# Optimization experiments

Hardware: AMD Instinct MI355X
Metric: run time of the kernel (lower is better)

## Reference

```python
import jax, jax.numpy as jnp
import numpy as np

B, N, L, S, H, E, D = 4, 32, 256, 256, 8, 64, 64

def setup_inputs() -> dict:
    key = jax.random.key(0)
    k1, k2, k3, k4 = jax.random.split(key, 4)
    queries = jax.random.normal(k1, (B, N, L, H, E), dtype=jnp.float32)
    keys = jax.random.normal(k2, (B, N, S, H, E), dtype=jnp.float32)
    values = jax.random.normal(k3, (B, N, S, H, D), dtype=jnp.float32)
    # additive causal mask [L, S]: 0 where allowed, -1e9 where masked
    causal = jnp.tril(jnp.ones((L, S), dtype=bool))
    attn_mask = jnp.where(causal, 0.0, -1e9).astype(jnp.float32)
    # cross-layer accumulated prior scores [B, N, H, L, S]
    attn_scores = jax.random.normal(k4, (B, N, H, L, S), dtype=jnp.float32) * 0.1
    query_lengths = jnp.full((B,), L, dtype=jnp.int32)
    key_lengths = jnp.full((B,), S, dtype=jnp.int32)
    return {"queries": queries, "keys": keys, "values": values,
            "attn_mask": attn_mask, "attn_scores": attn_scores,
            "query_lengths": query_lengths, "key_lengths": key_lengths}

def reference(queries, keys, values, attn_mask, attn_scores, query_lengths, key_lengths):
    # queries: [B,N,L,H,E], keys: [B,N,S,H,E], values: [B,N,S,H,D]
    e = queries.shape[-1]
    softmax_temp = 1.0 / np.sqrt(e).astype(np.float32)
    QK = jnp.einsum('bnlhe,bnshe->bnhls', queries, keys)
    # additive mask broadcast over [B,N,H]
    scores = QK + attn_mask + attn_scores  # accumulated scores returned for next layer
    A = jax.nn.softmax(softmax_temp * scores, axis=-1)  # dropout omitted (eval mode)
    V = jnp.einsum('bnhls,bnshd->bnlhd', A, values)
    return scores, V
```

## Files before the change

### kernel.cpp

```cpp
#include <hip/hip_runtime.h>
#include <stdint.h>


typedef __attribute__((ext_vector_type(8))) short bfrag;
typedef __attribute__((ext_vector_type(4))) float f32x4;
typedef __attribute__((ext_vector_type(4))) int i32x4;

__device__ __forceinline__ uint32_t f2bf(float f) {
  uint32_t u = __builtin_bit_cast(uint32_t, f);
  return (u + 0x7FFFu + ((u >> 16) & 1u)) >> 16;
}
__device__ __forceinline__ uint32_t pk(float a, float b) {
  return f2bf(a) | (f2bf(b) << 16);
}

#define MFMA(a, b, c) __builtin_amdgcn_mfma_f32_16x16x32_bf16((a), (b), (c), 0, 0, 0)

__global__ __launch_bounds__(1024, 2) void attn_kernel(
    const float* __restrict__ Qg, const float* __restrict__ Kg,
    const float* __restrict__ Vg, const float* __restrict__ Pg,
    float* __restrict__ Sc, float* __restrict__ Ov)
{
  __shared__ unsigned short Ks[256 * 72];
  __shared__ unsigned short Vt[64 * 266];

  const int bnh = blockIdx.x;
  const int bn = bnh >> 3, h = bnh & 7;
  const int t = threadIdx.x;

  {
    const int e0 = (t & 15) * 4;
    const int rb = t >> 4;
    const float* kp = Kg + (size_t)bn * 131072 + h * 64 + e0;
#pragma unroll
    for (int it = 0; it < 4; ++it) {
      const int r = it * 64 + rb;
      const f32x4 k4 = *(const f32x4*)(kp + (size_t)r * 512);
      uint2 kk;
      kk.x = pk(k4.x, k4.y);
      kk.y = pk(k4.z, k4.w);
      *(uint2*)(&Ks[r * 72 + e0]) = kk;
    }
  }
  {
    const int d = t & 63, sg = t >> 6;
    const float* vp = Vg + (size_t)bn * 131072 + h * 64 + d;
#pragma unroll
    for (int it = 0; it < 4; ++it) {
      const int sv = it * 64 + sg * 4;
      const float v0 = vp[(size_t)(sv + 0) * 512];
      const float v1 = vp[(size_t)(sv + 1) * 512];
      const float v2 = vp[(size_t)(sv + 2) * 512];
      const float v3 = vp[(size_t)(sv + 3) * 512];
      uint2 vv;
      vv.x = pk(v0, v1);
      vv.y = pk(v2, v3);
      *(uint2*)(&Vt[d * 266 + sv]) = vv;
    }
  }

  const int lane = t & 63;
  const int wave = t >> 6;
  const int ql = lane & 15;
  const int g  = lane >> 4;
  const int qbase = wave * 16;
  const int q = qbase + ql;
  const float temp = 0.125f;

  bfrag qf[2];
#pragma unroll
  for (int ks = 0; ks < 2; ++ks) {
    const float* qp = Qg + (size_t)bn * 131072 + (size_t)q * 512 + h * 64 + ks * 32 + g * 8;
    const f32x4 qa = *(const f32x4*)qp;
    const f32x4 qb = *(const f32x4*)(qp + 4);
    union { i32x4 i; bfrag b; } u;
    u.i = i32x4{(int)pk(qa.x, qa.y), (int)pk(qa.z, qa.w),
                (int)pk(qb.x, qb.y), (int)pk(qb.z, qb.w)};
    qf[ks] = u.b;
  }

  __syncthreads();

  f32x4 O[4];
#pragma unroll
  for (int ds = 0; ds < 4; ++ds) O[ds] = f32x4{0.f, 0.f, 0.f, 0.f};
  float m = -1e30f, lsum = 0.f;

  const size_t scb = (size_t)bnh << 16;
  const float* prp = Pg + scb + (size_t)q * 256 + 4 * g;
  float* scp = Sc + scb + (size_t)q * 256 + 4 * g;
  const int pvmax = wave >> 1;

  f32x4 pr0 = __builtin_nontemporal_load((const f32x4*)(prp));
  f32x4 pr1 = __builtin_nontemporal_load((const f32x4*)(prp + 16));

#pragma unroll 1
  for (int st = 0; st < 8; ++st) {
    const int s0 = st * 32;
    bfrag kf[2][2];
#pragma unroll
    for (int ss = 0; ss < 2; ++ss)
#pragma unroll
      for (int ks = 0; ks < 2; ++ks)
        kf[ss][ks] = *(const bfrag*)(&Ks[(s0 + 16 * ss + ql) * 72 + ks * 32 + g * 8]);

    f32x4 acc[2];
#pragma unroll
    for (int ss = 0; ss < 2; ++ss) {
      f32x4 a = f32x4{0.f, 0.f, 0.f, 0.f};
      a = MFMA(kf[ss][0], qf[0], a);
      a = MFMA(kf[ss][1], qf[1], a);
      const int sb = s0 + 16 * ss + 4 * g;
#pragma unroll
      for (int r = 0; r < 4; ++r)
        a[r] = (sb + r <= q) ? a[r] : a[r] - 1e9f;
      acc[ss] = a + (ss == 0 ? pr0 : pr1);
    }

    if (st < 7) {
      pr0 = __builtin_nontemporal_load((const f32x4*)(prp + (st + 1) * 32));
      pr1 = __builtin_nontemporal_load((const f32x4*)(prp + (st + 1) * 32 + 16));
    }

    __builtin_nontemporal_store(acc[0], (f32x4*)(scp + s0));
    __builtin_nontemporal_store(acc[1], (f32x4*)(scp + s0 + 16));

    if (st <= pvmax) {
      float tm = fmaxf(fmaxf(fmaxf(acc[0][0], acc[0][1]), fmaxf(acc[0][2], acc[0][3])),
                       fmaxf(fmaxf(acc[1][0], acc[1][1]), fmaxf(acc[1][2], acc[1][3])));
      tm = fmaxf(tm, __shfl_xor(tm, 16));
      tm = fmaxf(tm, __shfl_xor(tm, 32));
      tm *= temp;
      const float mnew = fmaxf(m, tm);
      const float fct = __expf(m - mnew);
      m = mnew;
      float p[8];
#pragma unroll
      for (int ss = 0; ss < 2; ++ss)
#pragma unroll
        for (int r = 0; r < 4; ++r)
          p[ss * 4 + r] = __expf(fmaf(temp, acc[ss][r], -mnew));
      float ts = (p[0] + p[1]) + (p[2] + p[3]) + (p[4] + p[5]) + (p[6] + p[7]);
      ts += __shfl_xor(ts, 16);
      ts += __shfl_xor(ts, 32);
      lsum = lsum * fct + ts;
#pragma unroll
      for (int ds = 0; ds < 4; ++ds) O[ds] *= fct;

      const int w0x = (int)pk(p[0], p[1]), w0y = (int)pk(p[2], p[3]);
      const int w1x = (int)pk(p[4], p[5]), w1y = (int)pk(p[6], p[7]);
      const int srcA = ((g & 1) << 5) + ql;
      const int a0 = __shfl(w0x, srcA),      a1 = __shfl(w1x, srcA);
      const int b0 = __shfl(w0y, srcA),      b1 = __shfl(w1y, srcA);
      const int c0 = __shfl(w0x, srcA + 16), c1 = __shfl(w1x, srcA + 16);
      const int d0 = __shfl(w0y, srcA + 16), d1 = __shfl(w1y, srcA + 16);
      union { i32x4 i; bfrag b; } pu;
      pu.i = i32x4{g < 2 ? a0 : a1, g < 2 ? b0 : b1,
                   g < 2 ? c0 : c1, g < 2 ? d0 : d1};

      bfrag vf[4];
#pragma unroll
      for (int ds = 0; ds < 4; ++ds)
        vf[ds] = *(const bfrag*)(&Vt[(16 * ds + ql) * 266 + s0 + g * 8]);
#pragma unroll
      for (int ds = 0; ds < 4; ++ds) O[ds] = MFMA(vf[ds], pu.b, O[ds]);
    }
  }

  {
    const float inv = 1.f / lsum;
    float* op = Ov + (size_t)bn * 131072 + (size_t)q * 512 + h * 64 + 4 * g;
#pragma unroll
    for (int ds = 0; ds < 4; ++ds) {
      f32x4 o = O[ds] * inv;
      *(f32x4*)(op + 16 * ds) = o;
    }
  }
}

extern "C" void kernel_launch(void* const* d_in, const int* in_sizes, int n_in,
                              void* d_out, int out_size, void* d_ws, size_t ws_size,
                              hipStream_t stream) {
  const float* Qg = (const float*)d_in[0];
  const float* Kg = (const float*)d_in[1];
  const float* Vg = (const float*)d_in[2];
  const float* Pg = (const float*)d_in[4];
  float* Sc = (float*)d_out;
  float* Ov = Sc + (size_t)4 * 32 * 8 * 256 * 256;
  attn_kernel<<<dim3(1024), dim3(1024), 0, stream>>>(Qg, Kg, Vg, Pg, Sc, Ov);
}
```

Baseline: 155.2 us.

## Stream K/V tiles through double-buffered swizzled LDS and balance causal waves

Replaces the up-front load of the full K and transposed V into large padded LDS arrays with per-step 32-row tiles. Each tile is converted to bf16 into a small double-buffered, XOR-swizzled LDS buffer while register prefetch fetches the next tile. A permutation table assigns query tiles to waves, and launch bounds are raised so far less LDS allows more resident blocks. This aims to hide global load latency behind compute and raise occupancy, at the cost of a barrier every iteration and tighter register limits.

New measurement: 288.2 us. 85.7% more time.

```diff
diff --git a/kernel.cpp b/kernel.cpp
--- a/kernel.cpp
+++ b/kernel.cpp
@@ -4,6 +4,7 @@
 
 typedef __attribute__((ext_vector_type(8))) short bfrag;
 typedef __attribute__((ext_vector_type(4))) float f32x4;
+typedef __attribute__((ext_vector_type(2))) float f32x2;
 typedef __attribute__((ext_vector_type(4))) int i32x4;
 
 __device__ __forceinline__ uint32_t f2bf(float f) {
@@ -16,56 +17,36 @@
 
 #define MFMA(a, b, c) __builtin_amdgcn_mfma_f32_16x16x32_bf16((a), (b), (c), 0, 0, 0)
 
-__global__ __launch_bounds__(1024, 2) void attn_kernel(
+__global__ __launch_bounds__(1024, 8) void attn_kernel(
     const float* __restrict__ Qg, const float* __restrict__ Kg,
     const float* __restrict__ Vg, const float* __restrict__ Pg,
     float* __restrict__ Sc, float* __restrict__ Ov)
 {
-  __shared__ unsigned short Ks[256 * 72];
-  __shared__ unsigned short Vt[64 * 266];
+  __shared__ char Kb[2][4096];
+  __shared__ char Vb[2][4096];
 
   const int bnh = blockIdx.x;
   const int bn = bnh >> 3, h = bnh & 7;
   const int t = threadIdx.x;
-
-  {
-    const int e0 = (t & 15) * 4;
-    const int rb = t >> 4;
-    const float* kp = Kg + (size_t)bn * 131072 + h * 64 + e0;
-#pragma unroll
-    for (int it = 0; it < 4; ++it) {
-      const int r = it * 64 + rb;
-      const f32x4 k4 = *(const f32x4*)(kp + (size_t)r * 512);
-      uint2 kk;
-      kk.x = pk(k4.x, k4.y);
-      kk.y = pk(k4.z, k4.w);
-      *(uint2*)(&Ks[r * 72 + e0]) = kk;
-    }
-  }
-  {
-    const int d = t & 63, sg = t >> 6;
-    const float* vp = Vg + (size_t)bn * 131072 + h * 64 + d;
-#pragma unroll
-    for (int it = 0; it < 4; ++it) {
-      const int sv = it * 64 + sg * 4;
-      const float v0 = vp[(size_t)(sv + 0) * 512];
-      const float v1 = vp[(size_t)(sv + 1) * 512];
-      const float v2 = vp[(size_t)(sv + 2) * 512];
-      const float v3 = vp[(size_t)(sv + 3) * 512];
-      uint2 vv;
-      vv.x = pk(v0, v1);
-      vv.y = pk(v2, v3);
-      *(uint2*)(&Vt[d * 266 + sv]) = vv;
-    }
-  }
-
   const int lane = t & 63;
   const int wave = t >> 6;
   const int ql = lane & 15;
   const int g  = lane >> 4;
-  const int qbase = wave * 16;
-  const int q = qbase + ql;
+  const int qt = (int)((0x783C96D25A1EB4F0ull >> (wave * 4)) & 15);
+  const int q = qt * 16 + ql;
+  const int pvmax = qt >> 1;
+  const int swzk = (ql & 7) << 4;
+  const int swzv = (ql & 3) << 4;
   const float temp = 0.125f;
+
+  const int kr_ = t >> 5;
+  const int kc_ = t & 31;
+  const int vd_ = t & 63;
+  const int vw_ = t >> 6;
+  const float* kgp = Kg + (size_t)bn * 131072 + h * 64 + (size_t)kr_ * 512 + 2 * kc_;
+  const float* vgp = Vg + (size_t)bn * 131072 + h * 64 + (size_t)(2 * vw_) * 512 + vd_;
+  const int kwoff = (kr_ * 128 + kc_ * 4) ^ ((kr_ & 7) << 4);
+  const int vwoff = (vd_ * 64 + vw_ * 4) ^ ((vd_ & 3) << 4);
 
   bfrag qf[2];
 #pragma unroll
@@ -79,7 +60,17 @@
     qf[ks] = u.b;
   }
 
-  __syncthreads();
+  f32x2 kreg = *(const f32x2*)kgp;
+  float vreg0 = vgp[0], vreg1 = vgp[512];
+  {
+    const uint32_t kk = pk(kreg[0], kreg[1]);
+    *(uint32_t*)(&Kb[0][0] + kwoff) = kk;
+    const uint32_t vv = pk(vreg0, vreg1);
+    *(uint32_t*)(&Vb[0][0] + vwoff) = vv;
+  }
+  kreg = *(const f32x2*)(kgp + 32 * 512);
+  vreg0 = vgp[16384];
+  vreg1 = vgp[16384 + 512];
 
   f32x4 O[4];
 #pragma unroll
@@ -89,20 +80,24 @@
   const size_t scb = (size_t)bnh << 16;
   const float* prp = Pg + scb + (size_t)q * 256 + 4 * g;
   float* scp = Sc + scb + (size_t)q * 256 + 4 * g;
-  const int pvmax = wave >> 1;
 
   f32x4 pr0 = __builtin_nontemporal_load((const f32x4*)(prp));
   f32x4 pr1 = __builtin_nontemporal_load((const f32x4*)(prp + 16));
+
+  asm volatile("s_waitcnt lgkmcnt(0)" ::: "memory");
+  __builtin_amdgcn_s_barrier();
 
 #pragma unroll 1
   for (int st = 0; st < 8; ++st) {
     const int s0 = st * 32;
+    const int p = (st & 1) << 12;
     bfrag kf[2][2];
 #pragma unroll
     for (int ss = 0; ss < 2; ++ss)
 #pragma unroll
       for (int ks = 0; ks < 2; ++ks)
-        kf[ss][ks] = *(const bfrag*)(&Ks[(s0 + 16 * ss + ql) * 72 + ks * 32 + g * 8]);
+        kf[ss][ks] = *(const bfrag*)(&Kb[0][0] + p +
+            (((16 * ss + ql) * 128 + ks * 64 + g * 16) ^ swzk));
 
     f32x4 acc[2];
 #pragma unroll
@@ -134,21 +129,21 @@
       const float mnew = fmaxf(m, tm);
       const float fct = __expf(m - mnew);
       m = mnew;
-      float p[8];
+      float pv[8];
 #pragma unroll
       for (int ss = 0; ss < 2; ++ss)
 #pragma unroll
         for (int r = 0; r < 4; ++r)
-          p[ss * 4 + r] = __expf(fmaf(temp, acc[ss][r], -mnew));
-      float ts = (p[0] + p[1]) + (p[2] + p[3]) + (p[4] + p[5]) + (p[6] + p[7]);
+          pv[ss * 4 + r] = __expf(fmaf(temp, acc[ss][r], -mnew));
+      float ts = (pv[0] + pv[1]) + (pv[2] + pv[3]) + (pv[4] + pv[5]) + (pv[6] + pv[7]);
       ts += __shfl_xor(ts, 16);
       ts += __shfl_xor(ts, 32);
       lsum = lsum * fct + ts;
 #pragma unroll
       for (int ds = 0; ds < 4; ++ds) O[ds] *= fct;
 
-      const int w0x = (int)pk(p[0], p[1]), w0y = (int)pk(p[2], p[3]);
-      const int w1x = (int)pk(p[4], p[5]), w1y = (int)pk(p[6], p[7]);
+      const int w0x = (int)pk(pv[0], pv[1]), w0y = (int)pk(pv[2], pv[3]);
+      const int w1x = (int)pk(pv[4], pv[5]), w1y = (int)pk(pv[6], pv[7]);
       const int srcA = ((g & 1) << 5) + ql;
       const int a0 = __shfl(w0x, srcA),      a1 = __shfl(w1x, srcA);
       const int b0 = __shfl(w0y, srcA),      b1 = __shfl(w1y, srcA);
@@ -161,10 +156,26 @@
       bfrag vf[4];
 #pragma unroll
       for (int ds = 0; ds < 4; ++ds)
-        vf[ds] = *(const bfrag*)(&Vt[(16 * ds + ql) * 266 + s0 + g * 8]);
+        vf[ds] = *(const bfrag*)(&Vb[0][0] + p +
+            (((16 * ds + ql) * 64 + g * 16) ^ swzv));
 #pragma unroll
       for (int ds = 0; ds < 4; ++ds) O[ds] = MFMA(vf[ds], pu.b, O[ds]);
     }
+
+    if (st < 7) {
+      const int p1 = ((st + 1) & 1) << 12;
+      const uint32_t kk = pk(kreg[0], kreg[1]);
+      *(uint32_t*)(&Kb[0][0] + p1 + kwoff) = kk;
+      const uint32_t vv = pk(vreg0, vreg1);
+      *(uint32_t*)(&Vb[0][0] + p1 + vwoff) = vv;
+      if (st < 6) {
+        kreg = *(const f32x2*)(kgp + (size_t)(st + 2) * 16384);
+        vreg0 = vgp[(st + 2) * 16384];
+        vreg1 = vgp[(st + 2) * 16384 + 512];
+      }
+    }
+    asm volatile("s_waitcnt lgkmcnt(0)" ::: "memory");
+    __builtin_amdgcn_s_barrier();
   }
 
   {
```
